# Performance work log

Hardware: AMD Instinct MI355X
Metric: run time of the kernel (lower is better)

Reference implementation:

```python
import jax, jax.numpy as jnp
import numpy as np

N, E, C, H, G, NC = 100000, 1600000, 128, 128, 256, 10
NEG_SLOPE = 0.2


def setup_inputs() -> dict:
    key = jax.random.key(0)
    ks = jax.random.split(key, 12)
    return {
        "x": jax.random.normal(ks[0], (N, C), jnp.float32),
        "edge_index": jax.random.randint(ks[1], (2, E), 0, N),
        "edge_attr": jax.random.uniform(ks[2], (E,), jnp.float32),
        "batch": jnp.sort(jax.random.randint(ks[3], (N,), 0, G)),
        "num_graphs": G,
        "att": jax.random.normal(ks[4], (3, 2 * C), jnp.float32) * (6.0 / (1 + 2 * C)) ** 0.5,
        "W1": jax.random.normal(ks[5], (3, C, H), jnp.float32) * (1.0 / C) ** 0.5,
        "b1": jnp.zeros((3, H), jnp.float32),
        "W2": jax.random.normal(ks[6], (3, H, H), jnp.float32) * (1.0 / H) ** 0.5,
        "b2": jnp.zeros((3, H), jnp.float32),
        "fc1_w": jax.random.normal(ks[7], (6 * H, 2 * H), jnp.float32) * (1.0 / (6 * H)) ** 0.5,
        "fc1_b": jnp.zeros((2 * H,), jnp.float32),
        "fc2_w": jax.random.normal(ks[8], (2 * H, H), jnp.float32) * (1.0 / (2 * H)) ** 0.5,
        "fc2_b": jnp.zeros((H,), jnp.float32),
        "fc3_w": jax.random.normal(ks[9], (H, NC), jnp.float32) * (1.0 / H) ** 0.5,
        "fc3_b": jnp.zeros((NC,), jnp.float32),
    }


def segment_sparsemax(z, seg, num_segments):
    """Exact sparsemax within each segment (ragged), vectorized via lexsort."""
    n = z.shape[0]
    order = jnp.lexsort((-z, seg))          # by segment asc, value desc
    zs, ss = z[order], seg[order]
    counts = jax.ops.segment_sum(jnp.ones((n,), jnp.int32), seg, num_segments)
    starts = jnp.cumsum(counts) - counts    # exclusive prefix -> segment start
    pos = jnp.arange(n, dtype=jnp.int32) - starts[ss]   # 0-based rank in segment
    ecs = jnp.cumsum(zs)
    base = jnp.concatenate([jnp.zeros((1,), zs.dtype), ecs])[starts[ss]]
    segcum = ecs - base                     # inclusive within-segment cumsum
    cond = 1.0 + (pos + 1).astype(zs.dtype) * zs > segcum  # support prefix mask
    k = jax.ops.segment_sum(cond.astype(zs.dtype), ss, num_segments)
    sum_k = jax.ops.segment_sum(jnp.where(cond, zs, 0.0), ss, num_segments)
    tau = jnp.where(k > 0, (sum_k - 1.0) / jnp.maximum(k, 1.0), 0.0)
    return jnp.maximum(z - tau[seg], 0.0)


def gcn_conv(x, row, col, ew, W, b, n_nodes):
    """PyG GCNConv with edge weights + self-loops (fill value 1)."""
    h = x @ W                                            # [N, H]
    deg = jax.ops.segment_sum(ew, col, n_nodes) + 1.0    # self-loop weight 1
    dinv = jnp.where(deg > 0, jax.lax.rsqrt(deg), 0.0)
    norm = dinv[row] * ew * dinv[col]                    # per-edge norm
    out = jax.ops.segment_sum(norm[:, None] * h[row], col, n_nodes)
    out = out + h * (dinv * dinv)[:, None]               # self-loop contribution
    return out + b


def emodel_block(x, row, col, att_b, W1_b, b1_b, W2_b, b2_b, n_nodes):
    # Edgelayer: att * cat([x[row], x[col]]) summed -> leaky_relu -> sparsemax(row)
    c = x.shape[1]
    s1 = x @ att_b[:c]                                   # [N]
    s2 = x @ att_b[c:]
    w = s1[row] + s2[col]
    w = jnp.where(w >= 0, w, NEG_SLOPE * w)              # leaky_relu
    p = segment_sparsemax(w, row, n_nodes)               # zero weight == pruned edge
    h = jax.nn.relu(gcn_conv(x, row, col, p, W1_b, b1_b, n_nodes))
    h = jax.nn.relu(gcn_conv(h, row, col, p, W2_b, b2_b, n_nodes))
    return h


def global_pools(z, batch, num_graphs):
    cnt = jax.ops.segment_sum(jnp.ones((z.shape[0], 1), z.dtype), batch, num_graphs)
    mean = jax.ops.segment_sum(z, batch, num_graphs) / jnp.maximum(cnt, 1.0)
    mx = jax.ops.segment_max(z, batch, num_graphs)
    mx = jnp.where(jnp.isfinite(mx), mx, 0.0)            # guard empty graphs
    return mean, mx


def reference(x, edge_index, edge_attr, batch, num_graphs, att, W1, b1, W2, b2,
              fc1_w, fc1_b, fc2_w, fc2_b, fc3_w, fc3_b):
    n_nodes = x.shape[0]
    row, col = edge_index[0], edge_index[1]
    feats = []
    for i in range(3):  # three structurally identical blocks with distinct params
        z = emodel_block(x, row, col, att[i], W1[i], b1[i], W2[i], b2[i], n_nodes)
        mean, mx = global_pools(z, batch, num_graphs)
        feats += [mean, mx]
    h = jnp.concatenate(feats, axis=1)                   # [G, 6*H]
    h = jax.nn.relu(h @ fc1_w + fc1_b)
    h = jax.nn.relu(h @ fc2_w + fc2_b)
    return jax.nn.log_softmax(h @ fc3_w + fc3_b, axis=-1)
```

## Files before the change

kernel.cpp:

```cpp
#include <hip/hip_runtime.h>
#include <math.h>

constexpr int NN   = 100000;
constexpr int EE   = 1600000;
constexpr int CH   = 128;
constexpr int GG   = 256;
constexpr int NCLS = 10;
constexpr int SW   = 48;
constexpr int QW   = 24;

constexpr int NB    = (NN + 63) >> 6;
constexpr int BCAP  = 1344;
constexpr int NCB   = (NN + 1023) >> 10;
constexpr int CBCAP = 18432;
constexpr int FPC   = 16;
constexpr int EPT  = 8;
constexpr int BINTB = 256;
constexpr int EPB  = BINTB * EPT;

typedef _Float16 half8  __attribute__((ext_vector_type(8)));
typedef _Float16 half4  __attribute__((ext_vector_type(4)));
typedef _Float16 half2v __attribute__((ext_vector_type(2)));
typedef float    float4v __attribute__((ext_vector_type(4)));

__global__ void bounds_kernel(const int* __restrict__ batch, int* __restrict__ gb,
                              int* __restrict__ ccur) {
    int t = blockIdx.x * blockDim.x + threadIdx.x;
    if (t < NCB) ccur[t] = 0;
    if (t > GG) return;
    int lo = 0, hi = NN;
    while (lo < hi) {
        int mid = (lo + hi) >> 1;
        if (batch[mid] < t) lo = mid + 1; else hi = mid;
    }
    gb[t] = lo;
}

__global__ void wt16_kernel(const float* __restrict__ W1, const float* __restrict__ W2,
                            _Float16* __restrict__ wt) {
    int mat = blockIdx.x;
    const float* src = (mat < 3) ? (W1 + (size_t)mat * 16384)
                                 : (W2 + (size_t)(mat - 3) * 16384);
    _Float16* dst = wt + (size_t)mat * 16384;
    for (int i = threadIdx.x; i < 16384; i += 256) {
        int n = i >> 7, k = i & 127;
        dst[n * 128 + k] = (_Float16)src[k * 128 + n];
    }
}

__global__ void scores3_kernel(const float* __restrict__ x, const float* __restrict__ att,
                               float* __restrict__ s1, float* __restrict__ s2,
                               int* __restrict__ cur, _Float16* __restrict__ x16) {
    int wid  = threadIdx.x >> 6;
    int lane = threadIdx.x & 63;
    int grp  = lane >> 4;
    int l16  = lane & 15;
    int node = blockIdx.x * 16 + wid * 4 + grp;
    if (node >= NN) return;
    const float4v* xp = (const float4v*)(x + (size_t)node * CH);
    float4v xa = xp[l16];
    float4v xb = xp[16 + l16];
    half4 ha, hb;
#pragma unroll
    for (int j = 0; j < 4; ++j) { ha[j] = (_Float16)xa[j]; hb[j] = (_Float16)xb[j]; }
    ((half4*)x16)[(size_t)node * 32 + l16]      = ha;
    ((half4*)x16)[(size_t)node * 32 + 16 + l16] = hb;
#pragma unroll
    for (int i = 0; i < 3; ++i) {
        const float* a = att + i * 256;
        float p1 = 0.f, p2 = 0.f;
#pragma unroll
        for (int j = 0; j < 4; ++j) {
            p1 += xa[j] * a[l16 * 4 + j];
            p1 += xb[j] * a[64 + l16 * 4 + j];
            p2 += xa[j] * a[128 + l16 * 4 + j];
            p2 += xb[j] * a[192 + l16 * 4 + j];
        }
#pragma unroll
        for (int off = 8; off > 0; off >>= 1) {
            p1 += __shfl_xor(p1, off, 64);
            p2 += __shfl_xor(p2, off, 64);
        }
        if (l16 == 0) { s1[i * NN + node] = p1; s2[i * NN + node] = p2; }
    }
    if (l16 == 0) {
        cur[node]          = 0;
        cur[NN + node]     = 0;
        cur[2 * NN + node] = 0;
    }
}

__global__ __launch_bounds__(256) void binc_kernel(const int* __restrict__ ei,
                                                   int* __restrict__ ccur,
                                                   unsigned int* __restrict__ coarse) {
    __shared__ int hist[NCB];
    __shared__ int basearr[NCB];
    int tid = threadIdx.x;
    if (tid < NCB) hist[tid] = 0;
    __syncthreads();
    int e0 = blockIdx.x * EPB;
    int r[EPT], c[EPT], off[EPT];
#pragma unroll
    for (int j = 0; j < EPT; ++j) {
        int e = e0 + j * BINTB + tid;
        if (e < EE) {
            r[j] = ei[e];
            c[j] = ei[EE + e];
            off[j] = atomicAdd(&hist[r[j] >> 10], 1);
        } else r[j] = -1;
    }
    __syncthreads();
    if (tid < NCB) {
        int n = hist[tid];
        basearr[tid] = n ? atomicAdd(&ccur[tid], n) : 0;
    }
    __syncthreads();
#pragma unroll
    for (int j = 0; j < EPT; ++j) {
        if (r[j] >= 0) {
            int b = r[j] >> 10;
            int pos = basearr[b] + off[j];
            if (pos < CBCAP)
                coarse[(size_t)b * CBCAP + pos] = (unsigned)(r[j] & 1023) | ((unsigned)c[j] << 10);
        }
    }
}

__global__ __launch_bounds__(512) void binf_kernel(const int* __restrict__ ccur,
                                                   const unsigned int* __restrict__ coarse,
                                                   int* __restrict__ bcur,
                                                   unsigned int* __restrict__ binned) {
    __shared__ int cnt2[FPC];
    int cb = blockIdx.x, tid = threadIdx.x;
    if (tid < FPC) cnt2[tid] = 0;
    __syncthreads();
    int cnt = min(ccur[cb], CBCAP);
    for (int idx = tid; idx < cnt; idx += 512) {
        unsigned u = coarse[(size_t)cb * CBCAP + idx];
        int fl = (u & 1023) >> 6;
        int pos = atomicAdd(&cnt2[fl], 1);
        if (pos < BCAP) {
            int fg = cb * FPC + fl;
            binned[(size_t)fg * BCAP + pos] = (u & 63) | ((u >> 10) << 6);
        }
    }
    __syncthreads();
    if (tid < FPC) {
        int fg = cb * FPC + tid;
        if (fg < NB) bcur[fg] = cnt2[tid];
    }
}

__global__ __launch_bounds__(512) void buildtau_kernel(const int* __restrict__ bcur,
                                                       const unsigned int* __restrict__ binned,
                                                       const float* __restrict__ s1,
                                                       const float* __restrict__ s2,
                                                       float* __restrict__ taubuf) {
    __shared__ int slot[64 * SW];
    __shared__ int cntl[64];
    __shared__ int listA[64], listB[64], listC[64];
    __shared__ int nA, nB, nC;
    int b   = blockIdx.x;
    int tid = threadIdx.x;
    if (tid < 64) cntl[tid] = 0;
    if (tid == 0) { nA = 0; nB = 0; nC = 0; }
    __syncthreads();
    int cnt = min(bcur[b], BCAP);
    for (int idx = tid; idx < cnt; idx += 512) {
        unsigned u = binned[(size_t)b * BCAP + idx];
        int rlo = u & 63;
        int p = atomicAdd(&cntl[rlo], 1);
        if (p < SW) slot[rlo * SW + p] = (int)(u >> 6);
    }
    __syncthreads();
    if (tid < 64) {
        int d = min(cntl[tid], SW);
        if (d > 0) {
            if (d <= 16)      listA[atomicAdd(&nA, 1)] = tid;
            else if (d <= 32) listB[atomicAdd(&nB, 1)] = tid;
            else              listC[atomicAdd(&nC, 1)] = tid;
        }
    }
    __syncthreads();
    int wid = tid >> 6, lane = tid & 63;
    const float NEGINF = __int_as_float(0xff800000);

    {
        int grp = lane >> 4, l16 = lane & 15;
        for (int ia = wid * 4; ia < nA; ia += 32) {
            int idx   = min(ia + grp, nA - 1);
            int myrlo = listA[idx];
            int mydeg = (ia + grp < nA) ? min(cntl[myrlo], SW) : 0;
            int vv    = (b << 6) + myrlo;
            int c = (l16 < mydeg) ? slot[myrlo * SW + l16] : 0;
            float z[3];
#pragma unroll
            for (int i = 0; i < 3; ++i) {
                z[i] = NEGINF;
                if (l16 < mydeg) {
                    float w = s1[i * NN + vv] + s2[i * NN + c];
                    z[i] = (w >= 0.f) ? w : 0.2f * w;
                }
            }
#pragma unroll
            for (int k = 2; k <= 16; k <<= 1) {
#pragma unroll
                for (int j = k >> 1; j > 0; j >>= 1) {
                    bool keepMax = ((l16 & j) == 0) == ((l16 & k) == 0);
#pragma unroll
                    for (int i = 0; i < 3; ++i) {
                        float other = __shfl_xor(z[i], j, 64);
                        z[i] = keepMax ? fmaxf(z[i], other) : fminf(z[i], other);
                    }
                }
            }
            float cs[3];
#pragma unroll
            for (int i = 0; i < 3; ++i) cs[i] = z[i];
#pragma unroll
            for (int off = 1; off < 16; off <<= 1) {
#pragma unroll
                for (int i = 0; i < 3; ++i) {
                    float t = __shfl_up(cs[i], off, 64);
                    if (l16 >= off) cs[i] += t;
                }
            }
#pragma unroll
            for (int i = 0; i < 3; ++i) {
                bool cond = (l16 < mydeg) && (1.f + (float)(l16 + 1) * z[i] > cs[i]);
                unsigned long long m = __ballot(cond);
                int myk = __popcll((m >> (grp * 16)) & 0xFFFFull);
                float sumk = __shfl(cs[i], grp * 16 + max(myk, 1) - 1, 64);
                if (l16 == 0 && mydeg > 0)
                    taubuf[i * NN + vv] = (sumk - 1.f) / (float)max(myk, 1);
            }
        }
    }

    {
        int half = lane >> 5, l32 = lane & 31;
        for (int ib = wid * 2; ib < nB; ib += 16) {
            int idx   = min(ib + half, nB - 1);
            int myrlo = listB[idx];
            int mydeg = (ib + half < nB) ? min(cntl[myrlo], SW) : 0;
            int vv    = (b << 6) + myrlo;
            int c = (l32 < mydeg) ? slot[myrlo * SW + l32] : 0;
            float z[3];
#pragma unroll
            for (int i = 0; i < 3; ++i) {
                z[i] = NEGINF;
                if (l32 < mydeg) {
                    float w = s1[i * NN + vv] + s2[i * NN + c];
                    z[i] = (w >= 0.f) ? w : 0.2f * w;
                }
            }
#pragma unroll
            for (int k = 2; k <= 32; k <<= 1) {
#pragma unroll
                for (int j = k >> 1; j > 0; j >>= 1) {
                    bool keepMax = ((l32 & j) == 0) == ((l32 & k) == 0);
#pragma unroll
                    for (int i = 0; i < 3; ++i) {
                        float other = __shfl_xor(z[i], j, 64);
                        z[i] = keepMax ? fmaxf(z[i], other) : fminf(z[i], other);
                    }
                }
            }
            float cs[3];
#pragma unroll
            for (int i = 0; i < 3; ++i) cs[i] = z[i];
#pragma unroll
            for (int off = 1; off < 32; off <<= 1) {
#pragma unroll
                for (int i = 0; i < 3; ++i) {
                    float t = __shfl_up(cs[i], off, 64);
                    if (l32 >= off) cs[i] += t;
                }
            }
#pragma unroll
            for (int i = 0; i < 3; ++i) {
                bool cond = (l32 < mydeg) && (1.f + (float)(l32 + 1) * z[i] > cs[i]);
                unsigned long long m = __ballot(cond);
                int myk = half ? __popcll(m >> 32) : __popcll(m & 0xFFFFFFFFull);
                float sumk = __shfl(cs[i], half * 32 + max(myk, 1) - 1, 64);
                if (l32 == 0 && mydeg > 0)
                    taubuf[i * NN + vv] = (sumk - 1.f) / (float)max(myk, 1);
            }
        }
    }

    for (int ic = wid; ic < nC; ic += 8) {
        int rlo = listC[ic];
        int deg = min(cntl[rlo], SW);
        int v   = (b << 6) + rlo;
        int c = (lane < deg) ? slot[rlo * SW + lane] : 0;
#pragma unroll
        for (int i = 0; i < 3; ++i) {
            float z = NEGINF;
            if (lane < deg) {
                float w = s1[i * NN + v] + s2[i * NN + c];
                z = (w >= 0.f) ? w : 0.2f * w;
            }
#pragma unroll
            for (int k = 2; k <= 64; k <<= 1) {
#pragma unroll
                for (int j = k >> 1; j > 0; j >>= 1) {
                    float other = __shfl_xor(z, j, 64);
                    bool keepMax = ((lane & j) == 0) == ((lane & k) == 0);
                    z = keepMax ? fmaxf(z, other) : fminf(z, other);
                }
            }
            float cs = z;
#pragma unroll
            for (int off = 1; off < 64; off <<= 1) {
                float t = __shfl_up(cs, off, 64);
                if (lane >= off) cs += t;
            }
            bool cond = (lane < deg) && (1.f + (float)(lane + 1) * z > cs);
            unsigned long long mask = __ballot(cond);
            int k = __popcll(mask);
            float sumk = __shfl(cs, k - 1, 64);
            if (lane == 0) taubuf[i * NN + v] = (sumk - 1.f) / (float)k;
        }
    }
}

__global__ void compact_kernel(const int* __restrict__ ei, const float* __restrict__ s1,
                               const float* __restrict__ s2, const float* __restrict__ taubuf,
                               int* __restrict__ qcnt, int2* __restrict__ qslot) {
    int e = blockIdx.x * blockDim.x + threadIdx.x;
    if (e >= EE) return;
    int r = ei[e], c = ei[EE + e];
    float w = s1[r] + s2[c];
    w = (w >= 0.f) ? w : 0.2f * w;
    float p = w - taubuf[r];
    if (p > 0.f) {
        int pos = atomicAdd(&qcnt[c], 1);
        if (pos < QW) qslot[c * QW + pos] = make_int2(r, __float_as_int(p));
    }
}

__global__ void degq_kernel(const int* __restrict__ qcnt, const int2* __restrict__ qslot,
                            float* __restrict__ dinv) {
    int v = blockIdx.x * blockDim.x + threadIdx.x;
    if (v >= NN) return;
    int cnt = min(qcnt[v], QW);
    double d = 1.0;
    int base = v * QW;
    for (int t = 0; t < cnt; ++t) d += (double)__int_as_float(qslot[base + t].y);
    dinv[v] = rsqrtf((float)d);
}

__global__ __launch_bounds__(256) void gemm16_kernel(const _Float16* __restrict__ A,
                                                     const _Float16* __restrict__ WT,
                                                     _Float16* __restrict__ Cout, int M) {
    int lane = threadIdx.x & 63;
    int wid  = threadIdx.x >> 6;
    int l15  = lane & 15;
    int quad = lane >> 4;
    int rowbase = blockIdx.x * 64 + wid * 16;
    int arow = rowbase + l15;

    float4v acc[8];
#pragma unroll
    for (int n = 0; n < 8; ++n) acc[n] = (float4v){0.f, 0.f, 0.f, 0.f};

#pragma unroll
    for (int kc = 0; kc < 4; ++kc) {
        half8 a = {};
        if (arow < M) a = *(const half8*)(A + (size_t)arow * CH + kc * 32 + quad * 8);
#pragma unroll
        for (int n = 0; n < 8; ++n) {
            half8 b = *(const half8*)(WT + (size_t)(n * 16 + l15) * CH + kc * 32 + quad * 8);
            acc[n] = __builtin_amdgcn_mfma_f32_16x16x32_f16(a, b, acc[n], 0, 0, 0);
        }
    }
#pragma unroll
    for (int n = 0; n < 8; ++n) {
#pragma unroll
        for (int r = 0; r < 4; ++r) {
            int row = rowbase + quad * 4 + r;
            if (row < M) Cout[(size_t)row * CH + n * 16 + l15] = (_Float16)acc[n][r];
        }
    }
}

__global__ void agg_kernel(const _Float16* __restrict__ hin,
                           const int* __restrict__ qcnt, const int2* __restrict__ qslot,
                           const float* __restrict__ dinv, const float* __restrict__ bias,
                           _Float16* __restrict__ out) {
    int wid  = threadIdx.x >> 6;
    int lane = threadIdx.x & 63;
    int grp  = lane >> 4;
    int l16  = lane & 15;
    int v = blockIdx.x * 16 + wid * 4 + grp;
    if (v >= NN) return;
    const half8* hin8 = (const half8*)hin;
    int cnt  = min(qcnt[v], QW);
    int base = v * QW;
    float dv = dinv[v];
    double acc[8];
#pragma unroll
    for (int j = 0; j < 8; ++j) acc[j] = 0.0;
    for (int t = 0; t < cnt; ++t) {
        int2 ep = qslot[base + t];
        int r = ep.x;
        float g = __int_as_float(ep.y) * dinv[r];
        half8 hr = hin8[(size_t)r * 16 + l16];
#pragma unroll
        for (int j = 0; j < 8; ++j)
            acc[j] += (double)g * (double)(float)hr[j];
    }
    half8 hv = hin8[(size_t)v * 16 + l16];
    const float* bp = bias + l16 * 8;
    half8 o;
#pragma unroll
    for (int j = 0; j < 8; ++j) {
        float oo = fmaxf(dv * (float)acc[j] + dv * dv * (float)hv[j] + bp[j], 0.f);
        o[j] = (_Float16)oo;
    }
    ((half8*)out)[(size_t)v * 16 + l16] = o;
}

__global__ void pool_kernel(const _Float16* __restrict__ z, const int* __restrict__ gb,
                            float* __restrict__ feats, int blk) {
    int g = blockIdx.x;
    int f = threadIdx.x;
    int s = gb[g], e = gb[g + 1];
    float sum = 0.f, mx = 0.f;
    const _Float16* zp = z + (size_t)s * CH + f;
    int n = s;
    for (; n + 16 <= e; n += 16) {
        float v[16];
#pragma unroll
        for (int j = 0; j < 16; ++j) v[j] = (float)zp[(size_t)j * CH];
#pragma unroll
        for (int j = 0; j < 16; ++j) {
            sum += v[j];
            mx = fmaxf(mx, v[j]);
        }
        zp += (size_t)16 * CH;
    }
    for (; n < e; ++n) {
        float v = (float)*zp;
        sum += v;
        mx = fmaxf(mx, v);
        zp += CH;
    }
    int cnt = e - s;
    feats[g * 768 + blk * 256 + f]       = sum / (float)max(cnt, 1);
    feats[g * 768 + blk * 256 + 128 + f] = mx;
}

__global__ void fc1_kernel(const float* __restrict__ feats, const float* __restrict__ w,
                           const float* __restrict__ b, float* __restrict__ t1) {
    __shared__ float lf[768];
    int g = blockIdx.x, j = threadIdx.x;
    for (int i = j; i < 768; i += 256) lf[i] = feats[g * 768 + i];
    __syncthreads();
    float acc = b[j];
    for (int k = 0; k < 768; ++k) acc += lf[k] * w[k * 256 + j];
    t1[g * 256 + j] = fmaxf(acc, 0.f);
}

__global__ void fc23_kernel(const float* __restrict__ t1,
                            const float* __restrict__ w2, const float* __restrict__ b2,
                            const float* __restrict__ w3, const float* __restrict__ b3,
                            float* __restrict__ out) {
    __shared__ float lt[256];
    __shared__ float lh[128];
    __shared__ float lg[NCLS];
    int g = blockIdx.x, j = threadIdx.x;
    lt[j]       = t1[g * 256 + j];
    lt[j + 128] = t1[g * 256 + 128 + j];
    __syncthreads();
    float acc = b2[j];
    for (int k = 0; k < 256; ++k) acc += lt[k] * w2[k * 128 + j];
    lh[j] = fmaxf(acc, 0.f);
    __syncthreads();
    if (j < NCLS) {
        float a = b3[j];
        for (int k = 0; k < 128; ++k) a += lh[k] * w3[k * NCLS + j];
        lg[j] = a;
    }
    __syncthreads();
    if (j == 0) {
        float mxv = lg[0];
        for (int i = 1; i < NCLS; ++i) mxv = fmaxf(mxv, lg[i]);
        float se = 0.f;
        for (int i = 0; i < NCLS; ++i) se += expf(lg[i] - mxv);
        float lse = logf(se) + mxv;
        for (int i = 0; i < NCLS; ++i) out[g * NCLS + i] = lg[i] - lse;
    }
}

extern "C" void kernel_launch(void* const* d_in, const int* in_sizes, int n_in,
                              void* d_out, int out_size, void* d_ws, size_t ws_size,
                              hipStream_t stream) {
    const float* x     = (const float*)d_in[0];
    const int*   ei    = (const int*)  d_in[1];
    const int*   batch = (const int*)  d_in[3];
    const float* att   = (const float*)d_in[5];
    const float* W1    = (const float*)d_in[6];
    const float* b1    = (const float*)d_in[7];
    const float* W2    = (const float*)d_in[8];
    const float* b2    = (const float*)d_in[9];
    const float* fc1w  = (const float*)d_in[10];
    const float* fc1b  = (const float*)d_in[11];
    const float* fc2w  = (const float*)d_in[12];
    const float* fc2b  = (const float*)d_in[13];
    const float* fc3w  = (const float*)d_in[14];
    const float* fc3b  = (const float*)d_in[15];
    float* out = (float*)d_out;

    char* p = (char*)d_ws;
    auto carve = [&](size_t bytes) -> void* {
        void* r = (void*)p;
        p += (bytes + 255) & ~(size_t)255;
        return r;
    };
    int* cur  = (int*)carve((size_t)3 * NN * 4);
    int* qcnt = cur;
    void* adj = carve((size_t)NN * QW * 8);
    unsigned int* binned = (unsigned int*)adj;
    unsigned int* coarse = binned + (size_t)NB * BCAP;
    int2*         qslot  = (int2*)adj;
    int* gb   = (int*)carve((size_t)(GG + 1) * 4);
    int* bcur = (int*)carve((size_t)NB * 4);
    int* ccur = (int*)carve((size_t)NCB * 4);
    float* s1     = (float*)carve((size_t)3 * NN * 4);
    float* s2     = (float*)carve((size_t)3 * NN * 4);
    float* taubuf = (float*)carve((size_t)3 * NN * 4);
    float* dinv   = (float*)carve((size_t)NN * 4);
    _Float16* wt16 = (_Float16*)carve((size_t)6 * 16384 * 2);
    _Float16* x16  = (_Float16*)carve((size_t)NN * CH * 2);
    _Float16* bufA = (_Float16*)carve((size_t)NN * CH * 2);
    _Float16* bufB = (_Float16*)carve((size_t)NN * CH * 2);
    float* feats  = (float*)carve((size_t)GG * 768 * 4);
    float* t1     = (float*)carve((size_t)GG * 256 * 4);

    const int TB = 256;
    dim3 egrid((EE + TB - 1) / TB);
    dim3 ngrid((NN + TB - 1) / TB);
    dim3 sgrid((NN + 15) / 16);
    dim3 ggrid((NN + 63) / 64);
    dim3 bingrid((EE + EPB - 1) / EPB);

    scores3_kernel<<<sgrid, 256, 0, stream>>>(x, att, s1, s2, cur, x16);
    bounds_kernel<<<2, 256, 0, stream>>>(batch, gb, ccur);
    binc_kernel<<<bingrid, BINTB, 0, stream>>>(ei, ccur, coarse);
    wt16_kernel<<<6, 256, 0, stream>>>(W1, W2, wt16);
    binf_kernel<<<NCB, 512, 0, stream>>>(ccur, coarse, bcur, binned);
    buildtau_kernel<<<NB, 512, 0, stream>>>(bcur, binned, s1, s2, taubuf);

    for (int i = 0; i < 3; ++i) {
        const float* s1_i  = s1 + (size_t)i * NN;
        const float* s2_i  = s2 + (size_t)i * NN;
        const float* tau_i = taubuf + (size_t)i * NN;
        int*         qc_i  = qcnt + (size_t)i * NN;
        const _Float16* WT1_i = wt16 + (size_t)i * 16384;
        const _Float16* WT2_i = wt16 + (size_t)(3 + i) * 16384;
        const float* b1_i  = b1 + i * CH;
        const float* b2_i  = b2 + i * CH;

        compact_kernel<<<egrid, TB, 0, stream>>>(ei, s1_i, s2_i, tau_i, qc_i, qslot);
        degq_kernel<<<ngrid, TB, 0, stream>>>(qc_i, qslot, dinv);

        gemm16_kernel<<<ggrid, 256, 0, stream>>>(x16, WT1_i, bufA, NN);
        agg_kernel<<<sgrid, 256, 0, stream>>>(bufA, qc_i, qslot, dinv, b1_i, bufB);
        gemm16_kernel<<<ggrid, 256, 0, stream>>>(bufB, WT2_i, bufA, NN);
        agg_kernel<<<sgrid, 256, 0, stream>>>(bufA, qc_i, qslot, dinv, b2_i, bufB);

        pool_kernel<<<GG, 128, 0, stream>>>(bufB, gb, feats, i);
    }

    fc1_kernel<<<GG, 256, 0, stream>>>(feats, fc1w, fc1b, t1);
    fc23_kernel<<<GG, 128, 0, stream>>>(t1, fc2w, fc2b, fc3w, fc3b, out);
}
```

Before: 834.3 us.

## Reuse row-binned edge list in compact kernel and widen per-node slot capacity

```diff
diff --git a/kernel.cpp b/kernel.cpp
--- a/kernel.cpp
+++ b/kernel.cpp
@@ -7,7 +7,7 @@
 constexpr int GG   = 256;
 constexpr int NCLS = 10;
 constexpr int SW   = 48;
-constexpr int QW   = 24;
+constexpr int QW   = 48;
 
 constexpr int NB    = (NN + 63) >> 6;
 constexpr int BCAP  = 1344;
@@ -325,18 +325,33 @@
     }
 }
 
-__global__ void compact_kernel(const int* __restrict__ ei, const float* __restrict__ s1,
-                               const float* __restrict__ s2, const float* __restrict__ taubuf,
-                               int* __restrict__ qcnt, int2* __restrict__ qslot) {
-    int e = blockIdx.x * blockDim.x + threadIdx.x;
-    if (e >= EE) return;
-    int r = ei[e], c = ei[EE + e];
-    float w = s1[r] + s2[c];
-    w = (w >= 0.f) ? w : 0.2f * w;
-    float p = w - taubuf[r];
-    if (p > 0.f) {
-        int pos = atomicAdd(&qcnt[c], 1);
-        if (pos < QW) qslot[c * QW + pos] = make_int2(r, __float_as_int(p));
+__global__ __launch_bounds__(512) void compact_kernel(const int* __restrict__ bcur,
+                                                      const unsigned int* __restrict__ binned,
+                                                      const float* __restrict__ s1,
+                                                      const float* __restrict__ s2,
+                                                      const float* __restrict__ taubuf,
+                                                      int* __restrict__ qcnt,
+                                                      int2* __restrict__ qslot) {
+    __shared__ float ls1[64], ltau[64];
+    int b = blockIdx.x, tid = threadIdx.x;
+    int rbase = b << 6;
+    if (tid < 64) {
+        int v = rbase + tid;
+        if (v < NN) { ls1[tid] = s1[v]; ltau[tid] = taubuf[v]; }
+    }
+    __syncthreads();
+    int cnt = min(bcur[b], BCAP);
+    for (int idx = tid; idx < cnt; idx += 512) {
+        unsigned u = binned[(size_t)b * BCAP + idx];
+        int rlo = u & 63;
+        int c   = (int)(u >> 6);
+        float w = ls1[rlo] + s2[c];
+        w = (w >= 0.f) ? w : 0.2f * w;
+        float p = w - ltau[rlo];
+        if (p > 0.f) {
+            int pos = atomicAdd(&qcnt[c], 1);
+            if (pos < QW) qslot[c * QW + pos] = make_int2(rbase + rlo, __float_as_int(p));
+        }
     }
 }
 
@@ -522,9 +537,9 @@
     int* cur  = (int*)carve((size_t)3 * NN * 4);
     int* qcnt = cur;
     void* adj = carve((size_t)NN * QW * 8);
-    unsigned int* binned = (unsigned int*)adj;
-    unsigned int* coarse = binned + (size_t)NB * BCAP;
+    unsigned int* coarse = (unsigned int*)adj;
     int2*         qslot  = (int2*)adj;
+    unsigned int* binned = (unsigned int*)carve((size_t)NB * BCAP * 4);
     int* gb   = (int*)carve((size_t)(GG + 1) * 4);
     int* bcur = (int*)carve((size_t)NB * 4);
     int* ccur = (int*)carve((size_t)NCB * 4);
@@ -540,7 +555,6 @@
     float* t1     = (float*)carve((size_t)GG * 256 * 4);
 
     const int TB = 256;
-    dim3 egrid((EE + TB - 1) / TB);
     dim3 ngrid((NN + TB - 1) / TB);
     dim3 sgrid((NN + 15) / 16);
     dim3 ggrid((NN + 63) / 64);
@@ -563,7 +577,8 @@
         const float* b1_i  = b1 + i * CH;
         const float* b2_i  = b2 + i * CH;
 
-        compact_kernel<<<egrid, TB, 0, stream>>>(ei, s1_i, s2_i, tau_i, qc_i, qslot);
+        compact_kernel<<<NB, 512, 0, stream>>>(bcur, binned, s1_i, s2_i, tau_i,
+                                               qc_i, qslot);
         degq_kernel<<<ngrid, TB, 0, stream>>>(qc_i, qslot, dinv);
 
         gemm16_kernel<<<ggrid, 256, 0, stream>>>(x16, WT1_i, bufA, NN);
```

Result: faster. 808.6 us (-3.1%).
